# Performance work log

Hardware: AMD Instinct MI355X
Metric: run time of the kernel (lower is better)

The kernel has to match this reference:

```python
import jax, jax.numpy as jnp
import numpy as np

B, T, K = 512, 1024, 48


def setup_inputs() -> dict:
    key = jax.random.key(0)
    k1, k2, k3, k4, k5, k6 = jax.random.split(key, 6)
    return {
        "emission_scores": jax.random.normal(k1, (B, T, K), dtype=jnp.float32),
        "lengths": jax.random.randint(k2, (B,), 1, T + 1, dtype=jnp.int64),
        "tags": jax.random.randint(k3, (B, T), 0, K, dtype=jnp.int64),
        "prior": 0.1 * jax.random.normal(k4, (K,), dtype=jnp.float32),
        "transition": 0.1 * jax.random.normal(k5, (K, K), dtype=jnp.float32),
        "final_transition": 0.1 * jax.random.normal(k6, (K,), dtype=jnp.float32),
    }


def _partition_function(emission_scores, lengths, prior, transition, final_transition):
    batch, timesteps, num_tags = emission_scores.shape
    # alpha_0[b, i] = emis[b, 0, i] + prior[i]
    alpha0 = emission_scores[:, 0, :] + prior[None, :]

    def step(prev_alpha, emis_t):
        # alpha_t[b, i] = logsumexp_j(prev_alpha[b, j] + transition[i, j]) + emis_t[b, i]
        a = jax.nn.logsumexp(prev_alpha[:, None, :] + transition[None, :, :], axis=2)
        a = a + emis_t
        return a, a

    emis_rest = jnp.swapaxes(emission_scores, 0, 1)[1:]  # [T-1, B, K]
    _, alphas = jax.lax.scan(step, alpha0, emis_rest)
    alphas = jnp.concatenate([alpha0[None], alphas], axis=0)  # [T, B, K]
    alpha_final = alphas[lengths - 1, jnp.arange(batch)]  # [B, K] at last valid step
    alpha_final = alpha_final + final_transition[None, :]
    return jax.nn.logsumexp(alpha_final, axis=1)


def _score_path(emission_scores, lengths, tags, prior, transition, final_transition):
    batch, timesteps, num_tags = emission_scores.shape
    emis_tag = jnp.take_along_axis(emission_scores, tags[:, :, None], axis=2)[..., 0]  # [B, T]
    trans = transition[tags[:, 1:], tags[:, :-1]]  # [B, T-1]
    pr = prior[tags[:, 0]][:, None]  # [B, 1]
    scores = jnp.concatenate([pr, trans], axis=1) + emis_tag  # [B, T]
    valid = jnp.arange(timesteps)[None, :] < lengths[:, None]  # True for t < length
    scores = jnp.where(valid, scores, 0.0)
    final_tags = tags[jnp.arange(batch), lengths - 1]
    return jnp.sum(scores, axis=1) + final_transition[final_tags]


def reference(emission_scores, lengths, tags, prior, transition, final_transition):
    lengths = jnp.clip(lengths, 1, None)
    logZ = _partition_function(emission_scores, lengths, prior, transition, final_transition)
    path = _score_path(emission_scores, lengths, tags, prior, transition, final_transition)
    return jnp.mean(logZ - path)
```

## Files before the change

### kernel.cpp

```cpp
#include <hip/hip_runtime.h>


#define BB    512
#define TT    1024
#define KK    48
#define GG    16
#define NGRP  32
#define NSLOT 16
#define SLOTB (13 * GG * 16)
#define PHASE 8
#define NPROD 3
#define BLKT  256

typedef __attribute__((ext_vector_type(4))) short bf16x4;
typedef __attribute__((ext_vector_type(4))) float f32x4;

__device__ __forceinline__ f32x4 mfma16(bf16x4 a, bf16x4 b, f32x4 c) {
#if __has_builtin(__builtin_amdgcn_mfma_f32_16x16x16bf16_1k)
    return __builtin_amdgcn_mfma_f32_16x16x16bf16_1k(a, b, c, 0, 0, 0);
#else
    f32x4 d;
    asm volatile("v_mfma_f32_16x16x16_bf16 %0, %1, %2, %3"
                 : "=v"(d) : "v"(a), "v"(b), "v"(c));
    return d;
#endif
}

#if __has_builtin(__builtin_amdgcn_cvt_pk_bf16_f32)
typedef __attribute__((ext_vector_type(2))) __bf16 bf16x2_v;
__device__ __forceinline__ unsigned pk2(float lo, float hi) {
    union { bf16x2_v v; unsigned u; } x;
    x.v = __builtin_amdgcn_cvt_pk_bf16_f32(lo, hi);
    return x.u;
}
#else
__device__ __forceinline__ unsigned pk2(float lo, float hi) {
    return __builtin_amdgcn_perm(__float_as_uint(hi) + 0x8000u,
                                 __float_as_uint(lo) + 0x8000u,
                                 0x07060302u);
}
#endif
__device__ __forceinline__ bf16x4 pack4(float a, float b, float c, float d) {
    union { unsigned u[2]; bf16x4 v; } x;
    x.u[0] = pk2(a, b);
    x.u[1] = pk2(c, d);
    return x.v;
}

__device__ __forceinline__ float wave_reduce_sum(float v) {
    #pragma unroll
    for (int off = 32; off > 0; off >>= 1)
        v += __shfl_xor(v, off, 64);
    return v;
}

__global__ __launch_bounds__(BLKT, 1) void crf_main_kernel(
    const float* __restrict__ emis,
    const int*   __restrict__ lengths,
    const int*   __restrict__ tags,
    const float* __restrict__ prior,
    const float* __restrict__ trans,
    const float* __restrict__ finalT,
    float*       __restrict__ ws)
{
    __shared__ __align__(16) unsigned char ring[NSLOT * SLOTB];
    __shared__ int prodCnt[NPROD];
    __shared__ int consCnt;

    const int tid  = threadIdx.x;
    const int wv   = tid >> 6;
    const int lane = tid & 63;

    if (blockIdx.x >= NGRP) {
        const int b = blockIdx.x - NGRP;
        int len = lengths[b];
        len = (len < 1) ? 1 : (len > TT ? TT : len);
        const float* eb = emis + (size_t)b * TT * KK;
        const int*   tg = tags + (size_t)b * TT;
        float ps = 0.0f;
        for (int t = tid; t < len; t += BLKT) {
            int cur = tg[t];
            float ev = eb[(size_t)t * KK + cur];
            float tr = (t == 0) ? prior[cur] : trans[cur * KK + tg[t - 1]];
            ps += ev + tr;
        }
        ps = wave_reduce_sum(ps);
        float* red = (float*)ring;
        if (lane == 0) red[wv] = ps;
        __syncthreads();
        if (tid == 0)
            ws[BB + b] = red[0] + red[1] + red[2] + red[3] + finalT[tg[len - 1]];
        return;
    }

    const int g = blockIdx.x;

    if (tid == 0) {
        prodCnt[0] = 0; prodCnt[1] = 0; prodCnt[2] = 0; consCnt = 0;
    }
    __syncthreads();

    int myLen = lengths[g * GG + (lane & 15)];
    myLen = (myLen < 1) ? 1 : (myLen > TT ? TT : myLen);
    int gmax = myLen;
    #pragma unroll
    for (int off = 32; off > 0; off >>= 1) {
        int o = __shfl_xor(gmax, off, 64);
        gmax = (o > gmax) ? o : gmax;
    }
    const int nsteps = gmax - 1;
    const int nphase = (nsteps + PHASE - 1) / PHASE;

    if (wv >= 1) {
        size_t go[3]; int lo16[3];
        #pragma unroll
        for (int j = 0; j < 3; ++j) {
            int lidx = lane + 64 * j;
            int s    = lidx / 12;
            int kg   = lidx - s * 12;
            go[j]    = (size_t)(g * GG + s) * (TT * KK) + kg * 4;
            lo16[j]  = (s * 13 + kg) * 16;
        }
        const int sA = wv - 1;
        float4 L[9];

#define PLOAD(KP)                                                          \
        {                                                                  \
            _Pragma("unroll")                                              \
            for (int h = 0; h < 3; ++h) {                                  \
                int s = sA + 3 * h;                                        \
                if (s < PHASE) {                                           \
                    int t  = 1 + (KP) * PHASE + s;                         \
                    int tc = (t > nsteps) ? nsteps : t;                    \
                    _Pragma("unroll")                                      \
                    for (int j = 0; j < 3; ++j)                            \
                        L[h*3+j] = *reinterpret_cast<const float4*>(       \
                            emis + go[j] + (size_t)tc * KK);               \
                }                                                          \
            }                                                              \
        }

        PLOAD(0);
        volatile int* vc = &consCnt;
        for (int k = 0; k < nphase; ++k) {
            while (*vc < k - 1) __builtin_amdgcn_s_sleep(1);
            asm volatile("" ::: "memory");
            #pragma unroll
            for (int h = 0; h < 3; ++h) {
                int s = sA + 3 * h;
                if (s < PHASE) {
                    int t = 1 + k * PHASE + s;
                    unsigned char* bp = &ring[(t & (NSLOT - 1)) * SLOTB];
                    #pragma unroll
                    for (int j = 0; j < 3; ++j) {
                        float4 l = L[h*3+j];
                        float4 e;
                        e.x = __expf(l.x); e.y = __expf(l.y);
                        e.z = __expf(l.z); e.w = __expf(l.w);
                        *reinterpret_cast<float4*>(bp + lo16[j]) = e;
                    }
                }
            }
            __threadfence_block();
            if (lane == 0) *(volatile int*)&prodCnt[sA] = k + 1;
            PLOAD(k + 1);
        }
#undef PLOAD
        return;
    }

    const int col   = lane & 15;
    const int grp   = lane >> 4;
    const int rbase = grp * 4;
    const int seq   = g * GG + col;
    const int lenn1 = myLen - 1;

    bf16x4 A[3][3];
    #pragma unroll
    for (int mt = 0; mt < 3; ++mt) {
        #pragma unroll
        for (int kt = 0; kt < 3; ++kt) {
            float4 tv = *reinterpret_cast<const float4*>(
                trans + (size_t)(mt * 16 + col) * KK + kt * 16 + rbase);
            A[mt][kt] = pack4(__expf(tv.x), __expf(tv.y),
                              __expf(tv.z), __expf(tv.w));
        }
    }

    float expF[12];
    #pragma unroll
    for (int mt = 0; mt < 3; ++mt) {
        float4 fv = *reinterpret_cast<const float4*>(finalT + mt * 16 + rbase);
        expF[mt*4+0] = __expf(fv.x); expF[mt*4+1] = __expf(fv.y);
        expF[mt*4+2] = __expf(fv.z); expF[mt*4+3] = __expf(fv.w);
    }

    const float* ebase = emis + (size_t)seq * TT * KK + rbase;

    float w[12];
    float c;
    float zcap = 0.0f;
    {
        float a0[12];
        #pragma unroll
        for (int mt = 0; mt < 3; ++mt) {
            float4 ev = *reinterpret_cast<const float4*>(ebase + mt * 16);
            float4 pv = *reinterpret_cast<const float4*>(prior + mt * 16 + rbase);
            a0[mt*4+0] = ev.x + pv.x;
            a0[mt*4+1] = ev.y + pv.y;
            a0[mt*4+2] = ev.z + pv.z;
            a0[mt*4+3] = ev.w + pv.w;
        }
        float mx = a0[0];
        #pragma unroll
        for (int r = 1; r < 12; ++r) mx = fmaxf(mx, a0[r]);
        mx = fmaxf(mx, __shfl_xor(mx, 16, 64));
        mx = fmaxf(mx, __shfl_xor(mx, 32, 64));
        c = mx;
        #pragma unroll
        for (int r = 0; r < 12; ++r) w[r] = __expf(a0[r] - c);
        if (__ballot(lenn1 == 0)) {
            float S = 0.0f;
            #pragma unroll
            for (int r = 0; r < 12; ++r) S = fmaf(w[r], expF[r], S);
            S += __shfl_xor(S, 16, 64);
            S += __shfl_xor(S, 32, 64);
            if (lenn1 == 0) zcap = c + __logf(S);
        }
    }

    bf16x4 Bt[3];
    Bt[0] = pack4(w[0], w[1], w[2],  w[3]);
    Bt[1] = pack4(w[4], w[5], w[6],  w[7]);
    Bt[2] = pack4(w[8], w[9], w[10], w[11]);

    const int foff = col * 52 + grp * 4;
    const f32x4 zero4 = {0.f, 0.f, 0.f, 0.f};
    volatile int* vp = prodCnt;

    for (int k = 0; k < nphase; ++k) {
        while (vp[0] < k + 1 || vp[1] < k + 1 || vp[2] < k + 1)
            __builtin_amdgcn_s_sleep(1);
        asm volatile("" ::: "memory");
        const int t0 = 1 + k * PHASE;
        const float* sp0 = reinterpret_cast<const float*>(
            &ring[(t0 & (NSLOT - 1)) * SLOTB]) + foff;
        float4 Xa = *reinterpret_cast<const float4*>(sp0);
        float4 Xb = *reinterpret_cast<const float4*>(sp0 + 16);
        float4 Xc = *reinterpret_cast<const float4*>(sp0 + 32);
        #pragma unroll
        for (int s8 = 0; s8 < PHASE; ++s8) {
            const int t = t0 + s8;
            float4 X0 = Xa, X1 = Xb, X2 = Xc;
            if (s8 + 1 < PHASE) {
                const float* spn = reinterpret_cast<const float*>(
                    &ring[((t + 1) & (NSLOT - 1)) * SLOTB]) + foff;
                Xa = *reinterpret_cast<const float4*>(spn);
                Xb = *reinterpret_cast<const float4*>(spn + 16);
                Xc = *reinterpret_cast<const float4*>(spn + 32);
            }

            f32x4 D0 = mfma16(A[0][0], Bt[0], zero4);
            f32x4 D1 = mfma16(A[1][0], Bt[0], zero4);
            f32x4 D2 = mfma16(A[2][0], Bt[0], zero4);
            D0 = mfma16(A[0][1], Bt[1], D0);
            D1 = mfma16(A[1][1], Bt[1], D1);
            D2 = mfma16(A[2][1], Bt[1], D2);
            D0 = mfma16(A[0][2], Bt[2], D0);
            D1 = mfma16(A[1][2], Bt[2], D1);
            D2 = mfma16(A[2][2], Bt[2], D2);

            w[0]  = D0.x * X0.x;  w[1]  = D0.y * X0.y;
            w[2]  = D0.z * X0.z;  w[3]  = D0.w * X0.w;
            w[4]  = D1.x * X1.x;  w[5]  = D1.y * X1.y;
            w[6]  = D1.z * X1.z;  w[7]  = D1.w * X1.w;
            w[8]  = D2.x * X2.x;  w[9]  = D2.y * X2.y;
            w[10] = D2.z * X2.z;  w[11] = D2.w * X2.w;

            if ((t & 7) == 0) {
                float mx = w[0];
                #pragma unroll
                for (int r = 1; r < 12; ++r) mx = fmaxf(mx, w[r]);
                mx = fmaxf(mx, __shfl_xor(mx, 16, 64));
                mx = fmaxf(mx, __shfl_xor(mx, 32, 64));
                c += __logf(mx);
                float rm = __builtin_amdgcn_rcpf(mx);
                #pragma unroll
                for (int r = 0; r < 12; ++r) w[r] *= rm;
            }

            if (__ballot(t == lenn1)) {
                float S = 0.0f;
                #pragma unroll
                for (int r = 0; r < 12; ++r) S = fmaf(w[r], expF[r], S);
                S += __shfl_xor(S, 16, 64);
                S += __shfl_xor(S, 32, 64);
                if (t == lenn1) zcap = c + __logf(S);
            }

            Bt[0] = pack4(w[0], w[1], w[2],  w[3]);
            Bt[1] = pack4(w[4], w[5], w[6],  w[7]);
            Bt[2] = pack4(w[8], w[9], w[10], w[11]);
        }
        __threadfence_block();
        asm volatile("" ::: "memory");
        if (lane == 0) *(volatile int*)&consCnt = k + 1;
    }

    if (lane < GG) ws[seq] = zcap;
}

__global__ __launch_bounds__(512) void reduce_mean_kernel(
    const float* __restrict__ ws, float* __restrict__ out)
{
    __shared__ float sm[8];
    int tid = threadIdx.x;
    float x = ws[tid] - ws[BB + tid];
    x = wave_reduce_sum(x);
    if ((tid & 63) == 0) sm[tid >> 6] = x;
    __syncthreads();
    if (tid < 8) {
        float y = sm[tid];
        y += __shfl_xor(y, 1, 64);
        y += __shfl_xor(y, 2, 64);
        y += __shfl_xor(y, 4, 64);
        if (tid == 0) out[0] = y * (1.0f / 512.0f);
    }
}

extern "C" void kernel_launch(void* const* d_in, const int* in_sizes, int n_in,
                              void* d_out, int out_size, void* d_ws, size_t ws_size,
                              hipStream_t stream) {
    const float* emis    = (const float*)d_in[0];
    const int*   lengths = (const int*)  d_in[1];
    const int*   tags    = (const int*)  d_in[2];
    const float* prior   = (const float*)d_in[3];
    const float* trans   = (const float*)d_in[4];
    const float* finalT  = (const float*)d_in[5];

    float* ws  = (float*)d_ws;
    float* out = (float*)d_out;

    crf_main_kernel<<<NGRP + BB, BLKT, 0, stream>>>(emis, lengths, tags, prior,
                                                    trans, finalT, ws);
    reduce_mean_kernel<<<1, 512, 0, stream>>>(ws, out);
}
```

Baseline: 331.1 us.

## Double-buffer producer loads, deepen consumer LDS prefetch, use permlane swaps for reductions

Producer waves now keep two register buffers of emission loads and alternate between them. This lets global loads run two phases ahead. The consumer unrolls two phases per iteration using compile-time ring slot bases, prefetches LDS two steps ahead, and releases its slot counter before the last step of each phase. The consumer also polls all producer counters with one vector load, raises wave priority with s_setprio, and uses permlane16/32 swap intrinsics for cross-lane max and sum. These changes target the serial latency of the recurrence chain, at the cost of more registers and more delicate signalling, since the slot is released early and fences are replaced by lgkmcnt waits.

After: 303.8 us. -8.2%, faster.

```diff
diff --git a/kernel.cpp b/kernel.cpp
--- a/kernel.cpp
+++ b/kernel.cpp
@@ -9,11 +9,11 @@
 #define NSLOT 16
 #define SLOTB (13 * GG * 16)
 #define PHASE 8
-#define NPROD 3
 #define BLKT  256
 
 typedef __attribute__((ext_vector_type(4))) short bf16x4;
 typedef __attribute__((ext_vector_type(4))) float f32x4;
+typedef __attribute__((ext_vector_type(4))) int   i32x4;
 
 __device__ __forceinline__ f32x4 mfma16(bf16x4 a, bf16x4 b, f32x4 c) {
 #if __has_builtin(__builtin_amdgcn_mfma_f32_16x16x16bf16_1k)
@@ -46,6 +46,37 @@
     x.u[1] = pk2(c, d);
     return x.v;
 }
+
+#if __has_builtin(__builtin_amdgcn_permlane16_swap)
+__device__ __forceinline__ float swap16_max(float x) {
+    auto p = __builtin_amdgcn_permlane16_swap(__float_as_int(x),
+                                              __float_as_int(x), false, false);
+    return fmaxf(__int_as_float(p[0]), __int_as_float(p[1]));
+}
+__device__ __forceinline__ float swap16_sum(float x) {
+    auto p = __builtin_amdgcn_permlane16_swap(__float_as_int(x),
+                                              __float_as_int(x), false, false);
+    return __int_as_float(p[0]) + __int_as_float(p[1]);
+}
+#else
+__device__ __forceinline__ float swap16_max(float x) { return fmaxf(x, __shfl_xor(x, 16, 64)); }
+__device__ __forceinline__ float swap16_sum(float x) { return x + __shfl_xor(x, 16, 64); }
+#endif
+#if __has_builtin(__builtin_amdgcn_permlane32_swap)
+__device__ __forceinline__ float swap32_max(float x) {
+    auto p = __builtin_amdgcn_permlane32_swap(__float_as_int(x),
+                                              __float_as_int(x), false, false);
+    return fmaxf(__int_as_float(p[0]), __int_as_float(p[1]));
+}
+__device__ __forceinline__ float swap32_sum(float x) {
+    auto p = __builtin_amdgcn_permlane32_swap(__float_as_int(x),
+                                              __float_as_int(x), false, false);
+    return __int_as_float(p[0]) + __int_as_float(p[1]);
+}
+#else
+__device__ __forceinline__ float swap32_max(float x) { return fmaxf(x, __shfl_xor(x, 32, 64)); }
+__device__ __forceinline__ float swap32_sum(float x) { return x + __shfl_xor(x, 32, 64); }
+#endif
 
 __device__ __forceinline__ float wave_reduce_sum(float v) {
     #pragma unroll
@@ -64,7 +95,7 @@
     float*       __restrict__ ws)
 {
     __shared__ __align__(16) unsigned char ring[NSLOT * SLOTB];
-    __shared__ int prodCnt[NPROD];
+    __shared__ __align__(16) int prodCnt4[4];
     __shared__ int consCnt;
 
     const int tid  = threadIdx.x;
@@ -94,9 +125,11 @@
     }
 
     const int g = blockIdx.x;
+    __builtin_amdgcn_s_setprio(1);
 
     if (tid == 0) {
-        prodCnt[0] = 0; prodCnt[1] = 0; prodCnt[2] = 0; consCnt = 0;
+        prodCnt4[0] = 0; prodCnt4[1] = 0; prodCnt4[2] = 0; prodCnt4[3] = 0;
+        consCnt = 0;
     }
     __syncthreads();
 
@@ -112,19 +145,19 @@
     const int nphase = (nsteps + PHASE - 1) / PHASE;
 
     if (wv >= 1) {
-        size_t go[3]; int lo16[3];
+        const float* gp[3]; int lo[3];
         #pragma unroll
         for (int j = 0; j < 3; ++j) {
             int lidx = lane + 64 * j;
             int s    = lidx / 12;
             int kg   = lidx - s * 12;
-            go[j]    = (size_t)(g * GG + s) * (TT * KK) + kg * 4;
-            lo16[j]  = (s * 13 + kg) * 16;
+            gp[j]    = emis + (size_t)(g * GG + s) * (TT * KK) + kg * 4;
+            lo[j]    = (s * 13 + kg) * 16;
         }
         const int sA = wv - 1;
-        float4 L[9];
-
-#define PLOAD(KP)                                                          \
+        float4 LA[9], LB[9];
+
+#define PLOADX(Lb, KP)                                                     \
         {                                                                  \
             _Pragma("unroll")                                              \
             for (int h = 0; h < 3; ++h) {                                  \
@@ -134,38 +167,55 @@
                     int tc = (t > nsteps) ? nsteps : t;                    \
                     _Pragma("unroll")                                      \
                     for (int j = 0; j < 3; ++j)                            \
-                        L[h*3+j] = *reinterpret_cast<const float4*>(       \
-                            emis + go[j] + (size_t)tc * KK);               \
+                        Lb[h * 3 + j] = *reinterpret_cast<const float4*>(  \
+                            gp[j] + (size_t)tc * KK);                      \
                 }                                                          \
             }                                                              \
         }
 
-        PLOAD(0);
+#define PSTORE(Lb, SB)                                                     \
+        {                                                                  \
+            _Pragma("unroll")                                              \
+            for (int h = 0; h < 3; ++h) {                                  \
+                int s = sA + 3 * h;                                        \
+                if (s < PHASE) {                                           \
+                    unsigned char* bp =                                    \
+                        &ring[(((SB) + s) & (NSLOT - 1)) * SLOTB];         \
+                    _Pragma("unroll")                                      \
+                    for (int j = 0; j < 3; ++j) {                          \
+                        float4 l = Lb[h * 3 + j];                          \
+                        float4 e;                                          \
+                        e.x = __expf(l.x); e.y = __expf(l.y);              \
+                        e.z = __expf(l.z); e.w = __expf(l.w);              \
+                        *reinterpret_cast<float4*>(bp + lo[j]) = e;        \
+                    }                                                      \
+                }                                                          \
+            }                                                              \
+        }
+
+        PLOADX(LA, 0);
+        PLOADX(LB, 1);
         volatile int* vc = &consCnt;
-        for (int k = 0; k < nphase; ++k) {
-            while (*vc < k - 1) __builtin_amdgcn_s_sleep(1);
+        for (int k0 = 0; k0 < nphase; k0 += 2) {
+            while (*vc < k0 - 1) __builtin_amdgcn_s_sleep(1);
             asm volatile("" ::: "memory");
-            #pragma unroll
-            for (int h = 0; h < 3; ++h) {
-                int s = sA + 3 * h;
-                if (s < PHASE) {
-                    int t = 1 + k * PHASE + s;
-                    unsigned char* bp = &ring[(t & (NSLOT - 1)) * SLOTB];
-                    #pragma unroll
-                    for (int j = 0; j < 3; ++j) {
-                        float4 l = L[h*3+j];
-                        float4 e;
-                        e.x = __expf(l.x); e.y = __expf(l.y);
-                        e.z = __expf(l.z); e.w = __expf(l.w);
-                        *reinterpret_cast<float4*>(bp + lo16[j]) = e;
-                    }
-                }
+            PSTORE(LA, 1);
+            asm volatile("s_waitcnt lgkmcnt(0)" ::: "memory");
+            if (lane == 0) *(volatile int*)&prodCnt4[sA] = k0 + 1;
+            asm volatile("" ::: "memory");
+            PLOADX(LA, k0 + 2);
+            if (k0 + 1 < nphase) {
+                while (*vc < k0) __builtin_amdgcn_s_sleep(1);
+                asm volatile("" ::: "memory");
+                PSTORE(LB, 9);
+                asm volatile("s_waitcnt lgkmcnt(0)" ::: "memory");
+                if (lane == 0) *(volatile int*)&prodCnt4[sA] = k0 + 2;
+                asm volatile("" ::: "memory");
+                PLOADX(LB, k0 + 3);
             }
-            __threadfence_block();
-            if (lane == 0) *(volatile int*)&prodCnt[sA] = k + 1;
-            PLOAD(k + 1);
-        }
-#undef PLOAD
+        }
+#undef PLOADX
+#undef PSTORE
         return;
     }
 
@@ -187,125 +237,128 @@
         }
     }
 
-    float expF[12];
+    f32x4 EF[3];
     #pragma unroll
     for (int mt = 0; mt < 3; ++mt) {
         float4 fv = *reinterpret_cast<const float4*>(finalT + mt * 16 + rbase);
-        expF[mt*4+0] = __expf(fv.x); expF[mt*4+1] = __expf(fv.y);
-        expF[mt*4+2] = __expf(fv.z); expF[mt*4+3] = __expf(fv.w);
+        EF[mt][0] = __expf(fv.x); EF[mt][1] = __expf(fv.y);
+        EF[mt][2] = __expf(fv.z); EF[mt][3] = __expf(fv.w);
     }
 
     const float* ebase = emis + (size_t)seq * TT * KK + rbase;
 
-    float w[12];
     float c;
     float zcap = 0.0f;
+    bf16x4 Bt0, Bt1, Bt2;
     {
-        float a0[12];
+        f32x4 a0[3];
         #pragma unroll
         for (int mt = 0; mt < 3; ++mt) {
-            float4 ev = *reinterpret_cast<const float4*>(ebase + mt * 16);
-            float4 pv = *reinterpret_cast<const float4*>(prior + mt * 16 + rbase);
-            a0[mt*4+0] = ev.x + pv.x;
-            a0[mt*4+1] = ev.y + pv.y;
-            a0[mt*4+2] = ev.z + pv.z;
-            a0[mt*4+3] = ev.w + pv.w;
-        }
-        float mx = a0[0];
-        #pragma unroll
-        for (int r = 1; r < 12; ++r) mx = fmaxf(mx, a0[r]);
-        mx = fmaxf(mx, __shfl_xor(mx, 16, 64));
-        mx = fmaxf(mx, __shfl_xor(mx, 32, 64));
+            f32x4 ev = *reinterpret_cast<const f32x4*>(ebase + mt * 16);
+            f32x4 pv = *reinterpret_cast<const f32x4*>(prior + mt * 16 + rbase);
+            a0[mt] = ev + pv;
+        }
+        float mx = fmaxf(
+            fmaxf(fmaxf(fmaxf(a0[0][0], a0[0][1]), fmaxf(a0[0][2], a0[0][3])),
+                  fmaxf(fmaxf(a0[1][0], a0[1][1]), fmaxf(a0[1][2], a0[1][3]))),
+            fmaxf(fmaxf(a0[2][0], a0[2][1]), fmaxf(a0[2][2], a0[2][3])));
+        mx = swap16_max(mx);
+        mx = swap32_max(mx);
         c = mx;
         #pragma unroll
-        for (int r = 0; r < 12; ++r) w[r] = __expf(a0[r] - c);
+        for (int mt = 0; mt < 3; ++mt) {
+            #pragma unroll
+            for (int e = 0; e < 4; ++e) a0[mt][e] = __expf(a0[mt][e] - c);
+        }
         if (__ballot(lenn1 == 0)) {
-            float S = 0.0f;
-            #pragma unroll
-            for (int r = 0; r < 12; ++r) S = fmaf(w[r], expF[r], S);
-            S += __shfl_xor(S, 16, 64);
-            S += __shfl_xor(S, 32, 64);
+            f32x4 Sv = a0[0] * EF[0] + a0[1] * EF[1] + a0[2] * EF[2];
+            float S = (Sv[0] + Sv[1]) + (Sv[2] + Sv[3]);
+            S = swap16_sum(S);
+            S = swap32_sum(S);
             if (lenn1 == 0) zcap = c + __logf(S);
         }
-    }
-
-    bf16x4 Bt[3];
-    Bt[0] = pack4(w[0], w[1], w[2],  w[3]);
-    Bt[1] = pack4(w[4], w[5], w[6],  w[7]);
-    Bt[2] = pack4(w[8], w[9], w[10], w[11]);
+        Bt0 = pack4(a0[0][0], a0[0][1], a0[0][2], a0[0][3]);
+        Bt1 = pack4(a0[1][0], a0[1][1], a0[1][2], a0[1][3]);
+        Bt2 = pack4(a0[2][0], a0[2][1], a0[2][2], a0[2][3]);
+    }
 
     const int foff = col * 52 + grp * 4;
     const f32x4 zero4 = {0.f, 0.f, 0.f, 0.f};
-    volatile int* vp = prodCnt;
-
-    for (int k = 0; k < nphase; ++k) {
-        while (vp[0] < k + 1 || vp[1] < k + 1 || vp[2] < k + 1)
-            __builtin_amdgcn_s_sleep(1);
-        asm volatile("" ::: "memory");
-        const int t0 = 1 + k * PHASE;
-        const float* sp0 = reinterpret_cast<const float*>(
-            &ring[(t0 & (NSLOT - 1)) * SLOTB]) + foff;
-        float4 Xa = *reinterpret_cast<const float4*>(sp0);
-        float4 Xb = *reinterpret_cast<const float4*>(sp0 + 16);
-        float4 Xc = *reinterpret_cast<const float4*>(sp0 + 32);
-        #pragma unroll
-        for (int s8 = 0; s8 < PHASE; ++s8) {
-            const int t = t0 + s8;
-            float4 X0 = Xa, X1 = Xb, X2 = Xc;
-            if (s8 + 1 < PHASE) {
-                const float* spn = reinterpret_cast<const float*>(
-                    &ring[((t + 1) & (NSLOT - 1)) * SLOTB]) + foff;
-                Xa = *reinterpret_cast<const float4*>(spn);
-                Xb = *reinterpret_cast<const float4*>(spn + 16);
-                Xc = *reinterpret_cast<const float4*>(spn + 32);
-            }
-
-            f32x4 D0 = mfma16(A[0][0], Bt[0], zero4);
-            f32x4 D1 = mfma16(A[1][0], Bt[0], zero4);
-            f32x4 D2 = mfma16(A[2][0], Bt[0], zero4);
-            D0 = mfma16(A[0][1], Bt[1], D0);
-            D1 = mfma16(A[1][1], Bt[1], D1);
-            D2 = mfma16(A[2][1], Bt[1], D2);
-            D0 = mfma16(A[0][2], Bt[2], D0);
-            D1 = mfma16(A[1][2], Bt[2], D1);
-            D2 = mfma16(A[2][2], Bt[2], D2);
-
-            w[0]  = D0.x * X0.x;  w[1]  = D0.y * X0.y;
-            w[2]  = D0.z * X0.z;  w[3]  = D0.w * X0.w;
-            w[4]  = D1.x * X1.x;  w[5]  = D1.y * X1.y;
-            w[6]  = D1.z * X1.z;  w[7]  = D1.w * X1.w;
-            w[8]  = D2.x * X2.x;  w[9]  = D2.y * X2.y;
-            w[10] = D2.z * X2.z;  w[11] = D2.w * X2.w;
-
-            if ((t & 7) == 0) {
-                float mx = w[0];
-                #pragma unroll
-                for (int r = 1; r < 12; ++r) mx = fmaxf(mx, w[r]);
-                mx = fmaxf(mx, __shfl_xor(mx, 16, 64));
-                mx = fmaxf(mx, __shfl_xor(mx, 32, 64));
-                c += __logf(mx);
-                float rm = __builtin_amdgcn_rcpf(mx);
-                #pragma unroll
-                for (int r = 0; r < 12; ++r) w[r] *= rm;
-            }
-
-            if (__ballot(t == lenn1)) {
-                float S = 0.0f;
-                #pragma unroll
-                for (int r = 0; r < 12; ++r) S = fmaf(w[r], expF[r], S);
-                S += __shfl_xor(S, 16, 64);
-                S += __shfl_xor(S, 32, 64);
-                if (t == lenn1) zcap = c + __logf(S);
-            }
-
-            Bt[0] = pack4(w[0], w[1], w[2],  w[3]);
-            Bt[1] = pack4(w[4], w[5], w[6],  w[7]);
-            Bt[2] = pack4(w[8], w[9], w[10], w[11]);
-        }
-        __threadfence_block();
-        asm volatile("" ::: "memory");
-        if (lane == 0) *(volatile int*)&consCnt = k + 1;
-    }
+
+#define XLOAD(dst, SLOT)                                                   \
+        {                                                                  \
+            const float* sp = reinterpret_cast<const float*>(              \
+                ring + (SLOT) * SLOTB) + foff;                             \
+            dst[0] = *reinterpret_cast<const f32x4*>(sp);                  \
+            dst[1] = *reinterpret_cast<const f32x4*>(sp + 16);             \
+            dst[2] = *reinterpret_cast<const f32x4*>(sp + 32);             \
+        }
+
+#define CPHASE(K_, SB)                                                       \
+    {                                                                        \
+        const int kc = (K_);                                                 \
+        for (;;) {                            \
+            i32x4 f = *(volatile i32x4*)prodCnt4;                            \
+            if (f[0] >= kc + 1 && f[1] >= kc + 1 && f[2] >= kc + 1) break;   \
+        }                                                                    \
+        asm volatile("" ::: "memory");                                       \
+        const int t0 = 1 + kc * PHASE;                                       \
+        f32x4 Xq[PHASE + 2][3];                                              \
+        XLOAD(Xq[0], ((SB) + 0) & (NSLOT - 1));                              \
+        XLOAD(Xq[1], ((SB) + 1) & (NSLOT - 1));                              \
+        _Pragma("unroll")                                                    \
+        for (int s8 = 0; s8 < PHASE; ++s8) {                                 \
+            if (s8 + 2 < PHASE)                        \
+                XLOAD(Xq[s8 + 2], ((SB) + s8 + 2) & (NSLOT - 1));            \
+            if (s8 == PHASE - 1) {                                           \
+                  \
+                asm volatile("s_waitcnt lgkmcnt(0)" ::: "memory");           \
+                if (lane == 0) *(volatile int*)&consCnt = kc + 1;            \
+                asm volatile("" ::: "memory");                               \
+            }                                                                \
+            const int t = t0 + s8;                \
+            f32x4 D0 = mfma16(A[0][0], Bt0, zero4);                          \
+            f32x4 D1 = mfma16(A[1][0], Bt0, zero4);                          \
+            f32x4 D2 = mfma16(A[2][0], Bt0, zero4);                          \
+            D0 = mfma16(A[0][1], Bt1, D0);                                   \
+            D1 = mfma16(A[1][1], Bt1, D1);                                   \
+            D2 = mfma16(A[2][1], Bt1, D2);                                   \
+            D0 = mfma16(A[0][2], Bt2, D0);                                   \
+            D1 = mfma16(A[1][2], Bt2, D1);                                   \
+            D2 = mfma16(A[2][2], Bt2, D2);                                   \
+            f32x4 Wa = D0 * Xq[s8][0];              \
+            f32x4 Wb = D1 * Xq[s8][1];                                       \
+            f32x4 Wc = D2 * Xq[s8][2];                                       \
+            if (s8 == PHASE - 1) {                    \
+                float mx = fmaxf(                                            \
+                    fmaxf(fmaxf(fmaxf(Wa[0], Wa[1]), fmaxf(Wa[2], Wa[3])),   \
+                          fmaxf(fmaxf(Wb[0], Wb[1]), fmaxf(Wb[2], Wb[3]))),  \
+                    fmaxf(fmaxf(Wc[0], Wc[1]), fmaxf(Wc[2], Wc[3])));        \
+                mx = swap16_max(mx);                                         \
+                mx = swap32_max(mx);                                         \
+                c += __logf(mx);                                             \
+                float rm = __builtin_amdgcn_rcpf(mx);                        \
+                Wa *= rm; Wb *= rm; Wc *= rm;                                \
+            }                                                                \
+            if (__ballot(t == lenn1)) {                    \
+                f32x4 Sv = Wa * EF[0] + Wb * EF[1] + Wc * EF[2];             \
+                float S = (Sv[0] + Sv[1]) + (Sv[2] + Sv[3]);                 \
+                S = swap16_sum(S);                                           \
+                S = swap32_sum(S);                                           \
+                if (t == lenn1) zcap = c + __logf(S);                        \
+            }                                                                \
+            Bt0 = pack4(Wa[0], Wa[1], Wa[2], Wa[3]);                         \
+            Bt1 = pack4(Wb[0], Wb[1], Wb[2], Wb[3]);                         \
+            Bt2 = pack4(Wc[0], Wc[1], Wc[2], Wc[3]);                         \
+        }                                                                    \
+    }
+
+    for (int k0 = 0; k0 < nphase; k0 += 2) {
+        CPHASE(k0, 1);
+        if (k0 + 1 < nphase) CPHASE(k0 + 1, 9);
+    }
+#undef CPHASE
+#undef XLOAD
 
     if (lane < GG) ws[seq] = zcap;
 }
```
